# Performance work log

Measured on AMD Instinct MI355X. Metric: run time of the kernel, lower is better.

The kernel has to match this reference:

```python
import jax, jax.numpy as jnp
import numpy as np

EPS = 1e-8  # torch F.cosine_similarity default eps


def setup_inputs() -> dict:
    key = jax.random.key(0)
    ks = jax.random.split(key, 8)
    B, N, D, H = 2, 256, 256, 8
    LEN = 2 * D + 4  # flag == 1
    query = jax.random.normal(ks[0], (B, N, N, D), dtype=jnp.float32)
    k_in = jax.random.normal(ks[1], (B, N, N, D), dtype=jnp.float32)
    s_query = jax.random.uniform(ks[2], (B, N, N, 2), dtype=jnp.float32)
    s_key = jax.random.uniform(ks[3], (B, N, N, 2), dtype=jnp.float32)
    roi_mask = jnp.ones((B, N, N), dtype=jnp.float32)
    # nn.Linear(LEN, H) params
    bound = 1.0 / np.sqrt(LEN)
    W = jax.random.uniform(ks[4], (H, LEN), minval=-bound, maxval=bound, dtype=jnp.float32)
    b_lin = jax.random.uniform(ks[5], (H,), minval=-bound, maxval=bound, dtype=jnp.float32)
    return {"query": query, "key": k_in, "s_query": s_query, "s_key": s_key,
            "roi_mask": roi_mask, "W": W, "b_lin": b_lin, "node_num": 32}


def reference(query, key, s_query, s_key, roi_mask, W, b_lin, node_num):
    B, N, _, D = query.shape
    # spatial feature for flag==1: simple concat
    spat = jnp.concatenate([s_query, s_key], axis=3)          # (B,N,N,4)
    ft = jnp.concatenate([query, key, spat], axis=3)          # (B,N,N,2D+4)
    attn1 = jax.nn.sigmoid(jnp.einsum('bqkc,hc->bqkh', ft, W) + b_lin)  # (B,N,N,H)

    # cosine-similarity scores over channel dim, then relu (Attention_4)
    qn = jnp.maximum(jnp.sqrt(jnp.sum(query * query, axis=3)), EPS)
    kn = jnp.maximum(jnp.sqrt(jnp.sum(key * key, axis=3)), EPS)
    scores = jnp.sum(query * key, axis=3) / (qn * kn)         # (B,N,N)
    attn = jax.nn.relu(scores)

    # torch: values, idces = topk(attn(B,N,N,1), node_num, dim=2);
    #        atten_mask[:, :, idces, :] = 1.0
    # Fancy indexing with the full idces tensor sets dim-2 position p to 1
    # for ALL (b, row) whenever p appears ANYWHERE in idces -> a global
    # indicator vector along dim 2.
    _, idces = jax.lax.top_k(attn, node_num)                  # (B,N,node_num)
    ind = jnp.zeros((N,), dtype=attn1.dtype).at[idces.reshape(-1)].set(1.0)

    out = attn1 * roi_mask[:, :, :, None] * ind[None, None, :, None]
    return out
```

## Files before the change

kernel.cpp:

```cpp
#include <hip/hip_runtime.h>
#include <hip/hip_bf16.h>

#define NPAIR 131072
#define NUNIT 8192
#define NH    8
#define NN    256
#define NROWS 512
#define LEN   516
#define EPSV  1e-8f

typedef __attribute__((ext_vector_type(8))) short bf16x8;
typedef __attribute__((ext_vector_type(4))) float f32x4;

__device__ __forceinline__ unsigned int pk2(float x, float y) {
    union { __hip_bfloat162 h; unsigned int u; } c;
    c.h = __float22bfloat162_rn(make_float2(x, y));
    return c.u;
}
__device__ __forceinline__ bf16x8 pack8(float4 a, float4 b) {
    union { unsigned int u[4]; bf16x8 v; } r;
    r.u[0] = pk2(a.x, a.y);
    r.u[1] = pk2(a.z, a.w);
    r.u[2] = pk2(b.x, b.y);
    r.u[3] = pk2(b.z, b.w);
    return r.v;
}

__global__ void fused_main(
    const float* __restrict__ Q, const float* __restrict__ K,
    const float* __restrict__ SQ, const float* __restrict__ SK,
    const float* __restrict__ ROI, const float* __restrict__ W,
    const float* __restrict__ Bb, float* __restrict__ out,
    float* __restrict__ scores)
{
    const int l    = threadIdx.x & 63;
    const int quad = l >> 4;
    const int m    = l & 15;
    const int hh   = m & 7;
    const int koff = quad * 8;
    const int nwaves = (gridDim.x * blockDim.x) >> 6;
    const int wave = (blockIdx.x * blockDim.x + threadIdx.x) >> 6;

    bf16x8 wqf[8], wkf[8];
#pragma unroll
    for (int c = 0; c < 8; ++c) {
        const float* wp = W + hh * LEN + c * 32 + koff;
        wqf[c] = pack8(*(const float4*)wp,        *(const float4*)(wp + 4));
        wkf[c] = pack8(*(const float4*)(wp + 256), *(const float4*)(wp + 260));
    }
    const float4 wt = *(const float4*)(W + hh * LEN + 512);
    const float bh = Bb[hh];

    const bool diag_owner = ((m >> 2) == quad);
    const int  dreg = m & 3;

    for (int u = wave; u < NUNIT; u += nwaves) {
        const int p0 = u * 16;
        const float* qbase = Q + (size_t)(p0 + m) * 256 + koff;
        const float* kbase = K + (size_t)(p0 + m) * 256 + koff;

        f32x4 a_qk = {0.f, 0.f, 0.f, 0.f};
        f32x4 a_qq = {0.f, 0.f, 0.f, 0.f};
        f32x4 a_kk = {0.f, 0.f, 0.f, 0.f};
        f32x4 a_pr = {0.f, 0.f, 0.f, 0.f};

#pragma unroll
        for (int c = 0; c < 8; ++c) {
            const float4 qa = *(const float4*)(qbase + c * 32);
            const float4 qb = *(const float4*)(qbase + c * 32 + 4);
            const float4 ka = *(const float4*)(kbase + c * 32);
            const float4 kb = *(const float4*)(kbase + c * 32 + 4);
            const bf16x8 qf = pack8(qa, qb);
            const bf16x8 kf = pack8(ka, kb);
            a_qk = __builtin_amdgcn_mfma_f32_16x16x32_bf16(qf, kf, a_qk, 0, 0, 0);
            a_qq = __builtin_amdgcn_mfma_f32_16x16x32_bf16(qf, qf, a_qq, 0, 0, 0);
            a_kk = __builtin_amdgcn_mfma_f32_16x16x32_bf16(kf, kf, a_kk, 0, 0, 0);
            a_pr = __builtin_amdgcn_mfma_f32_16x16x32_bf16(qf, wqf[c], a_pr, 0, 0, 0);
            a_pr = __builtin_amdgcn_mfma_f32_16x16x32_bf16(kf, wkf[c], a_pr, 0, 0, 0);
        }

        if (diag_owner) {
            const float qk = a_qk[dreg];
            const float qq = a_qq[dreg];
            const float kk = a_kk[dreg];
            const float d = fmaxf(sqrtf(qq), EPSV) * fmaxf(sqrtf(kk), EPSV);
            scores[p0 + m] = fmaxf(qk / d, 0.0f);
        }

        if (m < NH) {
#pragma unroll
            for (int r = 0; r < 4; ++r) {
                const int p = p0 + quad * 4 + r;
                const float2 sq = ((const float2*)SQ)[p];
                const float2 sk = ((const float2*)SK)[p];
                const float roi = ROI[p];
                const float x = a_pr[r] + sq.x * wt.x + sq.y * wt.y
                                        + sk.x * wt.z + sk.y * wt.w + bh;
                out[(size_t)p * NH + m] = roi / (1.0f + __expf(-x));
            }
        }
    }
}

__global__ void zero_ind(float* __restrict__ ind) {
    ind[threadIdx.x] = 0.0f;
}

__global__ __launch_bounds__(64) void topk_kernel(
    const float* __restrict__ scores, float* __restrict__ ind,
    const int* __restrict__ node_num)
{
    const int row = blockIdx.x;
    const int lane = threadIdx.x;
    const float4 v4 = *(const float4*)(scores + row * NN + lane * 4);
    float v[4] = {v4.x, v4.y, v4.z, v4.w};

    int Kk = node_num[0];
    if (Kk > NN) Kk = NN;
    for (int t = 0; t < Kk; t++) {
        float mv = v[0];
        int mi = lane * 4;
#pragma unroll
        for (int j = 1; j < 4; j++) {
            if (v[j] > mv) { mv = v[j]; mi = lane * 4 + j; }
        }
        for (int off = 32; off > 0; off >>= 1) {
            const float ov = __shfl_xor(mv, off, 64);
            const int   oi = __shfl_xor(mi, off, 64);
            if (ov > mv || (ov == mv && oi < mi)) { mv = ov; mi = oi; }
        }
        if (lane == 0) ind[mi] = 1.0f;
        if ((mi >> 2) == lane) v[mi & 3] = -1.0f;
    }
}

__global__ __launch_bounds__(256) void apply_ind_kernel(
    float* __restrict__ out, const float* __restrict__ ind)
{
    const int i = blockIdx.x * blockDim.x + threadIdx.x;
    float4 v = ((float4*)out)[i];
    const float m = ind[(i >> 1) & (NN - 1)];
    v.x *= m; v.y *= m; v.z *= m; v.w *= m;
    ((float4*)out)[i] = v;
}

extern "C" void kernel_launch(void* const* d_in, const int* in_sizes, int n_in,
                              void* d_out, int out_size, void* d_ws, size_t ws_size,
                              hipStream_t stream)
{
    const float* Q   = (const float*)d_in[0];
    const float* K   = (const float*)d_in[1];
    const float* SQ  = (const float*)d_in[2];
    const float* SK  = (const float*)d_in[3];
    const float* ROI = (const float*)d_in[4];
    const float* W   = (const float*)d_in[5];
    const float* Bb  = (const float*)d_in[6];
    const int* node_num = (const int*)d_in[7];

    float* out = (float*)d_out;
    float* scores = (float*)d_ws;
    float* ind = scores + NPAIR;

    fused_main<<<1024, 256, 0, stream>>>(Q, K, SQ, SK, ROI, W, Bb, out, scores);
    zero_ind<<<1, 256, 0, stream>>>(ind);
    topk_kernel<<<NROWS, 64, 0, stream>>>(scores, ind, node_num);
    apply_ind_kernel<<<out_size / 4 / 256, 256, 0, stream>>>(out, ind);
}
```

Before: 321.5 us.

## Double-buffer Q/K loads into LDS with async global_load_lds and fold zero_ind

The main kernel now stages Q and K quarter-rows through per-wave double-buffered LDS slots using global_load_lds, with a swizzled layout and explicit vmcnt waits. This overlaps memory traffic with MFMA work, and each wave owns a fixed set of four units. The grid is halved to 512 blocks, and the zero_ind kernel is folded into block 0 of the main kernel to save a launch. A risk is that ind is zeroed inside the main kernel while topk writes it later; that ordering holds because the kernels run on the same stream.

```diff
diff --git a/kernel.cpp b/kernel.cpp
--- a/kernel.cpp
+++ b/kernel.cpp
@@ -9,8 +9,14 @@
 #define LEN   516
 #define EPSV  1e-8f
 
+#define BLOCKS   512
+#define WAVES_PB 4
+#define UPW      4
+#define NQ       (UPW * 4)
+
 typedef __attribute__((ext_vector_type(8))) short bf16x8;
 typedef __attribute__((ext_vector_type(4))) float f32x4;
+typedef unsigned int u32;
 
 __device__ __forceinline__ unsigned int pk2(float x, float y) {
     union { __hip_bfloat162 h; unsigned int u; } c;
@@ -26,26 +32,36 @@
     return r.v;
 }
 
+__device__ __forceinline__ void gload16(const void* g, void* l) {
+    __builtin_amdgcn_global_load_lds(
+        (const __attribute__((address_space(1))) u32*)g,
+        (__attribute__((address_space(3))) u32*)l, 16, 0, 0);
+}
+
 __global__ void fused_main(
     const float* __restrict__ Q, const float* __restrict__ K,
     const float* __restrict__ SQ, const float* __restrict__ SK,
     const float* __restrict__ ROI, const float* __restrict__ W,
     const float* __restrict__ Bb, float* __restrict__ out,
-    float* __restrict__ scores)
-{
-    const int l    = threadIdx.x & 63;
+    float* __restrict__ scores, float* __restrict__ ind)
+{
+    __shared__ __align__(16) unsigned char lds[WAVES_PB][2][8192];
+
+    if (blockIdx.x == 0 && threadIdx.x < NN) ind[threadIdx.x] = 0.0f;
+
+    const int tid  = threadIdx.x;
+    const int wid  = tid >> 6;
+    const int l    = tid & 63;
     const int quad = l >> 4;
     const int m    = l & 15;
     const int hh   = m & 7;
-    const int koff = quad * 8;
-    const int nwaves = (gridDim.x * blockDim.x) >> 6;
-    const int wave = (blockIdx.x * blockDim.x + threadIdx.x) >> 6;
+    const int s7   = m & 7;
 
     bf16x8 wqf[8], wkf[8];
 #pragma unroll
     for (int c = 0; c < 8; ++c) {
-        const float* wp = W + hh * LEN + c * 32 + koff;
-        wqf[c] = pack8(*(const float4*)wp,        *(const float4*)(wp + 4));
+        const float* wp = W + hh * LEN + c * 32 + quad * 8;
+        wqf[c] = pack8(*(const float4*)wp,         *(const float4*)(wp + 4));
         wkf[c] = pack8(*(const float4*)(wp + 256), *(const float4*)(wp + 260));
     }
     const float4 wt = *(const float4*)(W + hh * LEN + 512);
@@ -54,56 +70,117 @@
     const bool diag_owner = ((m >> 2) == quad);
     const int  dreg = m & 3;
 
-    for (int u = wave; u < NUNIT; u += nwaves) {
-        const int p0 = u * 16;
-        const float* qbase = Q + (size_t)(p0 + m) * 256 + koff;
-        const float* kbase = K + (size_t)(p0 + m) * 256 + koff;
-
-        f32x4 a_qk = {0.f, 0.f, 0.f, 0.f};
-        f32x4 a_qq = {0.f, 0.f, 0.f, 0.f};
-        f32x4 a_kk = {0.f, 0.f, 0.f, 0.f};
-        f32x4 a_pr = {0.f, 0.f, 0.f, 0.f};
-
-#pragma unroll
-        for (int c = 0; c < 8; ++c) {
-            const float4 qa = *(const float4*)(qbase + c * 32);
-            const float4 qb = *(const float4*)(qbase + c * 32 + 4);
-            const float4 ka = *(const float4*)(kbase + c * 32);
-            const float4 kb = *(const float4*)(kbase + c * 32 + 4);
-            const bf16x8 qf = pack8(qa, qb);
-            const bf16x8 kf = pack8(ka, kb);
+    const int gw = blockIdx.x * WAVES_PB + wid;
+    const int u0 = gw * UPW;
+
+    const int smm = l >> 4;
+    const int slu = l & 15;
+
+    auto STAGE = [&](int t) {
+        const int un  = u0 + (t >> 2);
+        const int qtr = t & 3;
+        unsigned char* slot = &lds[wid][t & 1][0];
+#pragma unroll
+        for (int i = 0; i < 4; ++i) {
+            const int mm = i * 4 + smm;
+            const int fo = (slu ^ (mm & 7)) << 2;
+            const size_t rb = (size_t)(un * 16 + mm) * 256 + qtr * 64 + fo;
+            gload16(Q + rb, slot + i * 1024);
+            gload16(K + rb, slot + 4096 + i * 1024);
+        }
+    };
+
+    f32x4 a_qk = {0.f, 0.f, 0.f, 0.f};
+    f32x4 a_qq = {0.f, 0.f, 0.f, 0.f};
+    f32x4 a_kk = {0.f, 0.f, 0.f, 0.f};
+    f32x4 a_pr = {0.f, 0.f, 0.f, 0.f};
+
+    float2 esq[4], esk[4];
+    float  eroi[4];
+
+    STAGE(0);
+    STAGE(1);
+
+#pragma unroll
+    for (int t = 0; t < NQ; ++t) {
+        if (t == NQ - 1) { asm volatile("s_waitcnt vmcnt(0)" ::: "memory"); }
+        else             { asm volatile("s_waitcnt vmcnt(8)" ::: "memory"); }
+        __builtin_amdgcn_sched_barrier(0);
+
+        if ((t & 3) == 0 && m < NH) {
+            const int p0 = (u0 + (t >> 2)) * 16;
+#pragma unroll
+            for (int r = 0; r < 4; ++r) {
+                const int p = p0 + quad * 4 + r;
+                esq[r]  = ((const float2*)SQ)[p];
+                esk[r]  = ((const float2*)SK)[p];
+                eroi[r] = ROI[p];
+            }
+        }
+
+        unsigned char* slot = &lds[wid][t & 1][0];
+        const int b   = m * 256;
+        const int u00 = ((2 * quad + 0) ^ s7) << 4;
+        const int u01 = ((2 * quad + 1) ^ s7) << 4;
+        const int u10 = ((8 + 2 * quad + 0) ^ s7) << 4;
+        const int u11 = ((8 + 2 * quad + 1) ^ s7) << 4;
+        const float4 qr00 = *(const float4*)(slot + b + u00);
+        const float4 qr01 = *(const float4*)(slot + b + u01);
+        const float4 qr10 = *(const float4*)(slot + b + u10);
+        const float4 qr11 = *(const float4*)(slot + b + u11);
+        const float4 kr00 = *(const float4*)(slot + 4096 + b + u00);
+        const float4 kr01 = *(const float4*)(slot + 4096 + b + u01);
+        const float4 kr10 = *(const float4*)(slot + 4096 + b + u10);
+        const float4 kr11 = *(const float4*)(slot + 4096 + b + u11);
+        asm volatile("s_waitcnt lgkmcnt(0)" ::: "memory");
+        __builtin_amdgcn_sched_barrier(0);
+
+        if (t + 2 < NQ) STAGE(t + 2);
+
+        const int c0 = (t & 3) * 2;
+        {
+            const bf16x8 qf = pack8(qr00, qr01);
+            const bf16x8 kf = pack8(kr00, kr01);
             a_qk = __builtin_amdgcn_mfma_f32_16x16x32_bf16(qf, kf, a_qk, 0, 0, 0);
             a_qq = __builtin_amdgcn_mfma_f32_16x16x32_bf16(qf, qf, a_qq, 0, 0, 0);
             a_kk = __builtin_amdgcn_mfma_f32_16x16x32_bf16(kf, kf, a_kk, 0, 0, 0);
-            a_pr = __builtin_amdgcn_mfma_f32_16x16x32_bf16(qf, wqf[c], a_pr, 0, 0, 0);
-            a_pr = __builtin_amdgcn_mfma_f32_16x16x32_bf16(kf, wkf[c], a_pr, 0, 0, 0);
-        }
-
-        if (diag_owner) {
-            const float qk = a_qk[dreg];
-            const float qq = a_qq[dreg];
-            const float kk = a_kk[dreg];
-            const float d = fmaxf(sqrtf(qq), EPSV) * fmaxf(sqrtf(kk), EPSV);
-            scores[p0 + m] = fmaxf(qk / d, 0.0f);
-        }
-
-        if (m < NH) {
-#pragma unroll
-            for (int r = 0; r < 4; ++r) {
-                const int p = p0 + quad * 4 + r;
-                const float2 sq = ((const float2*)SQ)[p];
-                const float2 sk = ((const float2*)SK)[p];
-                const float roi = ROI[p];
-                const float x = a_pr[r] + sq.x * wt.x + sq.y * wt.y
-                                        + sk.x * wt.z + sk.y * wt.w + bh;
-                out[(size_t)p * NH + m] = roi / (1.0f + __expf(-x));
+            a_pr = __builtin_amdgcn_mfma_f32_16x16x32_bf16(qf, wqf[c0], a_pr, 0, 0, 0);
+            a_pr = __builtin_amdgcn_mfma_f32_16x16x32_bf16(kf, wkf[c0], a_pr, 0, 0, 0);
+        }
+        {
+            const bf16x8 qf = pack8(qr10, qr11);
+            const bf16x8 kf = pack8(kr10, kr11);
+            a_qk = __builtin_amdgcn_mfma_f32_16x16x32_bf16(qf, kf, a_qk, 0, 0, 0);
+            a_qq = __builtin_amdgcn_mfma_f32_16x16x32_bf16(qf, qf, a_qq, 0, 0, 0);
+            a_kk = __builtin_amdgcn_mfma_f32_16x16x32_bf16(kf, kf, a_kk, 0, 0, 0);
+            a_pr = __builtin_amdgcn_mfma_f32_16x16x32_bf16(qf, wqf[c0 + 1], a_pr, 0, 0, 0);
+            a_pr = __builtin_amdgcn_mfma_f32_16x16x32_bf16(kf, wkf[c0 + 1], a_pr, 0, 0, 0);
+        }
+
+        if ((t & 3) == 3) {
+            const int p0 = (u0 + (t >> 2)) * 16;
+            if (diag_owner) {
+                const float qk = a_qk[dreg];
+                const float qq = a_qq[dreg];
+                const float kk = a_kk[dreg];
+                const float d = fmaxf(sqrtf(qq), EPSV) * fmaxf(sqrtf(kk), EPSV);
+                scores[p0 + m] = fmaxf(qk / d, 0.0f);
             }
+            if (m < NH) {
+#pragma unroll
+                for (int r = 0; r < 4; ++r) {
+                    const int p = p0 + quad * 4 + r;
+                    const float x = a_pr[r] + esq[r].x * wt.x + esq[r].y * wt.y
+                                            + esk[r].x * wt.z + esk[r].y * wt.w + bh;
+                    out[(size_t)p * NH + m] = eroi[r] / (1.0f + __expf(-x));
+                }
+            }
+            a_qk = {0.f, 0.f, 0.f, 0.f};
+            a_qq = {0.f, 0.f, 0.f, 0.f};
+            a_kk = {0.f, 0.f, 0.f, 0.f};
+            a_pr = {0.f, 0.f, 0.f, 0.f};
         }
     }
-}
-
-__global__ void zero_ind(float* __restrict__ ind) {
-    ind[threadIdx.x] = 0.0f;
 }
 
 __global__ __launch_bounds__(64) void topk_kernel(
@@ -161,8 +238,8 @@
     float* scores = (float*)d_ws;
     float* ind = scores + NPAIR;
 
-    fused_main<<<1024, 256, 0, stream>>>(Q, K, SQ, SK, ROI, W, Bb, out, scores);
-    zero_ind<<<1, 256, 0, stream>>>(ind);
+    fused_main<<<BLOCKS, 256, 0, stream>>>(Q, K, SQ, SK, ROI, W, Bb, out,
+                                           scores, ind);
     topk_kernel<<<NROWS, 64, 0, stream>>>(scores, ind, node_num);
     apply_ind_kernel<<<out_size / 4 / 256, 256, 0, stream>>>(out, ind);
 }
```

Result: slower. 343.6 us (+6.9%).
